# Kernel optimization log

Measured on AMD Instinct MI355X. Metric: run time of the kernel, lower is better.

Reference implementation:

```python
import jax, jax.numpy as jnp
import numpy as np

D_INNER = 1024
D_STATE = 16
DT_RANK = 64


def setup_inputs() -> dict:
    key = jax.random.key(0)
    k1, k2, k3, k4 = jax.random.split(key, 4)
    B, T = 8, 2048
    x = jax.random.normal(k1, (B, T, D_INNER), dtype=jnp.float32)
    pad_mask = jnp.zeros((B, T), dtype=bool)
    # nn.Linear weights: out = x @ W.T
    Wxp = 0.02 * jax.random.normal(k2, (DT_RANK + 2 * D_STATE, D_INNER), dtype=jnp.float32)
    Wdt = 0.02 * jax.random.normal(k3, (D_INNER, DT_RANK), dtype=jnp.float32)
    bdt = 0.02 * jax.random.normal(k4, (D_INNER,), dtype=jnp.float32)
    # log_A init: log(arange(1..d_state)) expanded to (d_inner, d_state)
    log_A = jnp.broadcast_to(jnp.log(jnp.arange(1, D_STATE + 1, dtype=jnp.float32))[None, :],
                             (D_INNER, D_STATE)).copy()
    D_param = jnp.ones((D_INNER,), dtype=jnp.float32)
    return {"x": x, "pad_mask": pad_mask, "Wxp": Wxp, "Wdt": Wdt, "bdt": bdt,
            "log_A": log_A, "D_param": D_param}


def reference(x, pad_mask, Wxp, Wdt, bdt, log_A, D_param):
    B, T, Din = x.shape
    xp = jnp.einsum('btd,kd->btk', x, Wxp)                      # (B,T,dt_rank+2N)
    dt = jax.nn.softplus(jnp.einsum('btr,dr->btd', xp[..., :DT_RANK], Wdt) + bdt)  # (B,T,Din)
    B_seq = xp[..., DT_RANK:DT_RANK + D_STATE]                  # (B,T,N)
    C_seq = xp[..., DT_RANK + D_STATE:]                         # (B,T,N)
    A = -jnp.exp(log_A)                                         # (Din,N)
    mask = (~pad_mask).astype(x.dtype)                          # (B,T), 1 = keep

    def step(h, inp):
        dt_t, B_t, C_t, x_t, m = inp   # (B,Din),(B,N),(B,N),(B,Din),(B,)
        dA = jnp.exp(A[None] * dt_t[..., None])                 # (B,Din,N)
        h = dA * h + (dt_t * x_t)[..., None] * B_t[:, None, :]  # (B,Din,N)
        y = jnp.einsum('bdn,bn->bd', h, C_t) + D_param * x_t
        y = y * m[:, None]
        h = h * m[:, None, None]
        return h, y

    h0 = jnp.zeros((B, Din, D_STATE), x.dtype)
    xs = (jnp.swapaxes(dt, 0, 1), jnp.swapaxes(B_seq, 0, 1),
          jnp.swapaxes(C_seq, 0, 1), jnp.swapaxes(x, 0, 1), mask.T)
    _, ys = jax.lax.scan(step, h0, xs)                          # ys: (T,B,Din)
    return jnp.swapaxes(ys, 0, 1)
```

## Files before the change

### kernel.cpp

```cpp
#include <hip/hip_runtime.h>
#include <stdint.h>

#define DIN 1024
#define TLEN 2048
#define NCH 16
#define CHT 128
#define WIN 32

typedef __attribute__((ext_vector_type(8))) short bf16x8;
typedef __attribute__((ext_vector_type(4))) float f32x4;

__device__ __forceinline__ short f2bf_trunc(float f) {
  union { float f; uint32_t u; } v; v.f = f;
  return (short)(v.u >> 16);
}
__device__ __forceinline__ short f2bf_rne(float f) {
  union { float f; uint32_t u; } v; v.f = f;
  uint32_t r = v.u + 0x7FFFu + ((v.u >> 16) & 1u);
  return (short)(r >> 16);
}
__device__ __forceinline__ float bf2f(short s) {
  union { uint32_t u; float f; } v; v.u = ((uint32_t)(unsigned short)s) << 16;
  return v.f;
}
__device__ __forceinline__ uint32_t pack_bf2(float a, float b) {
  union { float f; uint32_t u; } va, vb; va.f = a; vb.f = b;
  return (va.u >> 16) | (vb.u & 0xFFFF0000u);
}
__device__ __forceinline__ float softplus_f(float v) {
  float e = __builtin_amdgcn_exp2f(v * 1.44269504f);
  float sp = __builtin_amdgcn_logf(1.0f + e) * 0.6931471806f;
  return v > 15.0f ? v : sp;
}
__device__ __forceinline__ void gl_lds16(const void* g, void* l) {
  __builtin_amdgcn_global_load_lds(
      (const __attribute__((address_space(1))) uint32_t*)g,
      (__attribute__((address_space(3))) uint32_t*)l, 16, 0, 0);
}
__device__ __forceinline__ f32x4 mfma16(bf16x8 a, bf16x8 b, f32x4 c) {
  return __builtin_amdgcn_mfma_f32_16x16x32_bf16(a, b, c, 0, 0, 0);
}
template <int CTRL>
__device__ __forceinline__ float dpp_add(float v) {
  int r = __builtin_amdgcn_update_dpp(0, __builtin_bit_cast(int, v), CTRL, 0xF, 0xF, 0);
  return v + __builtin_bit_cast(float, r);
}

__global__ void k_prep(const float* __restrict__ Wxp, const float* __restrict__ Wdt,
                       const float* __restrict__ logA, const unsigned char* __restrict__ pad,
                       short* __restrict__ wxp_bf, short* __restrict__ wdt_bf,
                       float* __restrict__ al2, uint32_t* __restrict__ padbits) {
  int i = blockIdx.x * 256 + threadIdx.x;
  if (i < 96 * 1024) wxp_bf[i] = f2bf_rne(Wxp[i]);
  if (i < 1024 * 64) wdt_bf[i] = f2bf_rne(Wdt[i]);
  if (i < 1024 * 16) al2[i] = -__expf(logA[i]) * 1.44269504f;
  if (i < 512) {
    uint32_t m = 0;
    const unsigned char* p = pad + (size_t)i * 32;
    for (int j = 0; j < 32; ++j) m |= (p[j] ? 1u : 0u) << j;
    padbits[i] = m;
  }
}

__global__ __launch_bounds__(256) void k_proj(
    const float* __restrict__ x, const short* __restrict__ wxp_bf,
    short* __restrict__ xp_dt, float* __restrict__ BC) {
  const int w = threadIdx.x >> 6, l = threadIdx.x & 63;
  const int cl = l & 15, q = l >> 4, kb = q * 8;
  const int rh = w & 1, ch = w >> 1;
  const int xrow = blockIdx.x * 32 + rh * 16 + cl;

  f32x4 acc[3];
#pragma unroll
  for (int t = 0; t < 3; ++t) acc[t] = (f32x4){0.f, 0.f, 0.f, 0.f};

  const float* xr = x + (size_t)xrow * DIN + kb;
  const short* wb = wxp_bf + (size_t)(ch * 48 + cl) * DIN + kb;
#pragma unroll 2
  for (int k0 = 0; k0 < DIN; k0 += 32) {
    float4 p0 = *(const float4*)(xr + k0);
    float4 p1 = *(const float4*)(xr + k0 + 4);
    bf16x8 xb;
    xb[0] = f2bf_trunc(p0.x); xb[1] = f2bf_trunc(p0.y);
    xb[2] = f2bf_trunc(p0.z); xb[3] = f2bf_trunc(p0.w);
    xb[4] = f2bf_trunc(p1.x); xb[5] = f2bf_trunc(p1.y);
    xb[6] = f2bf_trunc(p1.z); xb[7] = f2bf_trunc(p1.w);
#pragma unroll
    for (int t = 0; t < 3; ++t) {
      bf16x8 wf = *(const bf16x8*)(wb + (size_t)t * 16 * DIN + k0);
      acc[t] = mfma16(wf, xb, acc[t]);
    }
  }
#pragma unroll
  for (int t = 0; t < 3; ++t) {
    int oc = ch * 48 + t * 16 + q * 4;
    if (oc < 64) {
      uint2 uu;
      uu.x = pack_bf2(acc[t][0], acc[t][1]);
      uu.y = pack_bf2(acc[t][2], acc[t][3]);
      *(uint2*)(xp_dt + (size_t)xrow * 64 + oc) = uu;
    } else {
      *(f32x4*)(BC + (size_t)xrow * 32 + (oc - 64)) = acc[t];
    }
  }
}

__global__ __launch_bounds__(256) void k_scan1(
    const float* __restrict__ x, const float* __restrict__ BC,
    const short* __restrict__ xp_dt, const short* __restrict__ wdt_bf,
    const float* __restrict__ bdt, const float* __restrict__ al2,
    const float* __restrict__ Dparam, const uint32_t* __restrict__ padbits,
    float* __restrict__ Y, float* __restrict__ Ssum, short* __restrict__ Hfin) {
  __shared__ float x_w[2][33 * 64];
  __shared__ float bc_w[2][33 * 32];
  __shared__ float dt_w[2][33 * 68];

  const int tid = threadIdx.x;
  const int w = tid >> 6, l = tid & 63;
  const int cl = l & 15, q = l >> 4, kb = q * 8;
  const int dg = blockIdx.x & 15;
  const int chunk = (blockIdx.x >> 4) & 15;
  const int b = blockIdx.x >> 8;
  const int d0 = dg * 64;
  const int cb = chunk * CHT;
  const int grp = tid >> 2, l2 = tid & 3, n0 = l2 * 4;
  const int d = d0 + grp;

  const f32x4 cA = *(const f32x4*)(al2 + (size_t)d * 16 + n0);
  const float Dp = Dparam[d];

  const int th = w & 1, dh = w >> 1;
  const short* wr0 = wdt_bf + (size_t)(d0 + dh * 32 + cl) * 64 + kb;
  const short* wr1 = wdt_bf + (size_t)(d0 + dh * 32 + 16 + cl) * 64 + kb;
  bf16x8 aw00 = *(const bf16x8*)(wr0);
  bf16x8 aw01 = *(const bf16x8*)(wr0 + 32);
  bf16x8 aw10 = *(const bf16x8*)(wr1);
  bf16x8 aw11 = *(const bf16x8*)(wr1 + 32);
  f32x4 bias0 = *(const f32x4*)(bdt + d0 + dh * 32 + q * 4);
  f32x4 bias1 = *(const f32x4*)(bdt + d0 + dh * 32 + 16 + q * 4);

  float h[4] = {0.f, 0.f, 0.f, 0.f};
  float S = 0.f;

  auto stage = [&](int t0, int buf) {
    const float* xg = x + ((size_t)(b * TLEN + t0)) * DIN + d0;
#pragma unroll
    for (int r = 0; r < 2; ++r) {
      int flat = r * 1024 + w * 256 + l * 4;
      int tt = flat >> 6, cc = flat & 63;
      gl_lds16(xg + (size_t)tt * DIN + cc, &x_w[buf][r * 1024 + w * 256]);
    }
    const float* bg = BC + ((size_t)(b * TLEN + t0)) * 32;
    gl_lds16(bg + w * 256 + l * 4, &bc_w[buf][w * 256]);
  };

  auto dtc = [&](int t0, int buf) {
    uint32_t mw = padbits[b * 64 + (t0 >> 5)];
    int tloc = th * 16 + cl;
    bool masked = (mw >> tloc) & 1;
    const short* ag = xp_dt + (size_t)(b * TLEN + t0 + tloc) * 64 + kb;
    bf16x8 b0 = *(const bf16x8*)(ag);
    bf16x8 b1 = *(const bf16x8*)(ag + 32);
    f32x4 ac = mfma16(aw00, b0, (f32x4){0.f, 0.f, 0.f, 0.f});
    ac = mfma16(aw01, b1, ac);
    f32x4 dv;
#pragma unroll
    for (int i = 0; i < 4; ++i) {
      float sp = softplus_f(ac[i] + bias0[i]);
      dv[i] = masked ? 1e9f : sp;
    }
    *(f32x4*)&dt_w[buf][tloc * 68 + dh * 32 + q * 4] = dv;
    ac = mfma16(aw10, b0, (f32x4){0.f, 0.f, 0.f, 0.f});
    ac = mfma16(aw11, b1, ac);
#pragma unroll
    for (int i = 0; i < 4; ++i) {
      float sp = softplus_f(ac[i] + bias1[i]);
      dv[i] = masked ? 1e9f : sp;
    }
    *(f32x4*)&dt_w[buf][tloc * 68 + dh * 32 + 16 + q * 4] = dv;
  };

  stage(cb, 0);
  dtc(cb, 0);
  __syncthreads();

  for (int win = 0; win < CHT / WIN; ++win) {
    const int curb = win & 1;
    const int t0 = cb + win * WIN;
    if (win < CHT / WIN - 1) { stage(t0 + WIN, curb ^ 1); dtc(t0 + WIN, curb ^ 1); }

    float* ybase = Y + ((size_t)(b * TLEN + t0)) * DIN + d;
    float dtv = dt_w[curb][grp];
    float xv = x_w[curb][grp];
    f32x4 Bv = *(const f32x4*)&bc_w[curb][n0];
    f32x4 Cv = *(const f32x4*)&bc_w[curb][16 + n0];
#pragma unroll 8
    for (int tt = 0; tt < WIN; ++tt) {
      float dtv_n = dt_w[curb][(tt + 1) * 68 + grp];
      float xv_n = x_w[curb][(tt + 1) * 64 + grp];
      f32x4 Bv_n = *(const f32x4*)&bc_w[curb][(tt + 1) * 32 + n0];
      f32x4 Cv_n = *(const f32x4*)&bc_w[curb][(tt + 1) * 32 + 16 + n0];

      bool live = dtv < 1e8f;
      float dtx = live ? dtv * xv : 0.f;
#pragma unroll
      for (int n = 0; n < 4; ++n) {
        float e = __builtin_amdgcn_exp2f(cA[n] * dtv);
        h[n] = fmaf(e, h[n], dtx * Bv[n]);
      }
      float p = h[0] * Cv[0];
      p = fmaf(h[1], Cv[1], p);
      p = fmaf(h[2], Cv[2], p);
      p = fmaf(h[3], Cv[3], p);
      p = dpp_add<0xB1>(p);
      p = dpp_add<0x4E>(p);
      S += dtv;
      float yv = live ? fmaf(Dp, xv, p) : 0.f;
      if (l2 == 0) ybase[(size_t)tt * DIN] = yv;

      dtv = dtv_n; xv = xv_n; Bv = Bv_n; Cv = Cv_n;
    }
    __syncthreads();
  }

  if (l2 == 0) Ssum[(size_t)(b * NCH + chunk) * 1024 + d] = S;
  short4 hs;
  hs.x = f2bf_rne(h[0]); hs.y = f2bf_rne(h[1]);
  hs.z = f2bf_rne(h[2]); hs.w = f2bf_rne(h[3]);
  *(short4*)(Hfin + ((size_t)(b * NCH + chunk) * 1024 + d) * 16 + n0) = hs;
}

__global__ __launch_bounds__(256) void k_fix(
    const float* __restrict__ BC, const short* __restrict__ xp_dt,
    const short* __restrict__ wdt_bf, const float* __restrict__ bdt,
    const float* __restrict__ al2, const uint32_t* __restrict__ padbits,
    const float* __restrict__ Ssum, const short* __restrict__ Hfin,
    float* __restrict__ Y) {
  __shared__ float dtw[32 * 260];
  __shared__ float c_w[32 * 16];

  const int tid = threadIdx.x;
  const int w = tid >> 6, l = tid & 63;
  const int cl = l & 15, q = l >> 4, kb = q * 8;
  const int b = blockIdx.x / 60;
  const int rem = blockIdx.x % 60;
  const int chunk = (rem >> 2) + 1;
  const int dblk = rem & 3;
  const int d = dblk * 256 + tid;
  const int th = w & 1, dh = w >> 1;

  float cA[16], hin[16];
#pragma unroll
  for (int g = 0; g < 4; ++g)
    *(f32x4*)&cA[g * 4] = *(const f32x4*)(al2 + (size_t)d * 16 + g * 4);
#pragma unroll
  for (int n = 0; n < 16; ++n) hin[n] = 0.f;

  for (int c = 0; c < chunk; ++c) {
    float s = Ssum[(size_t)(b * NCH + c) * 1024 + d];
    const short4* hp = (const short4*)(Hfin + ((size_t)(b * NCH + c) * 1024 + d) * 16);
#pragma unroll
    for (int g = 0; g < 4; ++g) {
      short4 hv = hp[g];
      hin[g * 4 + 0] = fmaf(__builtin_amdgcn_exp2f(cA[g * 4 + 0] * s), hin[g * 4 + 0], bf2f(hv.x));
      hin[g * 4 + 1] = fmaf(__builtin_amdgcn_exp2f(cA[g * 4 + 1] * s), hin[g * 4 + 1], bf2f(hv.y));
      hin[g * 4 + 2] = fmaf(__builtin_amdgcn_exp2f(cA[g * 4 + 2] * s), hin[g * 4 + 2], bf2f(hv.z));
      hin[g * 4 + 3] = fmaf(__builtin_amdgcn_exp2f(cA[g * 4 + 3] * s), hin[g * 4 + 3], bf2f(hv.w));
    }
  }

  float S = 0.f;
  for (int win = 0; win < CHT / WIN; ++win) {
    const int t0 = chunk * CHT + win * WIN;
    __syncthreads();
    if (w == 0) {
      gl_lds16(BC + ((size_t)(b * TLEN + t0 + (l >> 2))) * 32 + 16 + (l & 3) * 4, &c_w[0]);
      gl_lds16(BC + ((size_t)(b * TLEN + t0 + 16 + (l >> 2))) * 32 + 16 + (l & 3) * 4, &c_w[256]);
    }
    uint32_t mw = padbits[b * 64 + (t0 >> 5)];
    const int tloc = th * 16 + cl;
    const bool masked = (mw >> tloc) & 1;
    const short* ag = xp_dt + (size_t)(b * TLEN + t0 + tloc) * 64 + kb;
    bf16x8 xb0 = *(const bf16x8*)(ag);
    bf16x8 xb1 = *(const bf16x8*)(ag + 32);
#pragma unroll
    for (int dti = 0; dti < 8; ++dti) {
      int dd = dh * 128 + dti * 16;
      const short* wr = wdt_bf + (size_t)(dblk * 256 + dd + cl) * 64 + kb;
      bf16x8 a0 = *(const bf16x8*)(wr);
      bf16x8 a1 = *(const bf16x8*)(wr + 32);
      f32x4 ac = mfma16(a0, xb0, (f32x4){0.f, 0.f, 0.f, 0.f});
      ac = mfma16(a1, xb1, ac);
      f32x4 bv = *(const f32x4*)(bdt + dblk * 256 + dd + q * 4);
      f32x4 dv;
#pragma unroll
      for (int i = 0; i < 4; ++i) {
        float sp = softplus_f(ac[i] + bv[i]);
        dv[i] = masked ? 1e9f : sp;
      }
      *(f32x4*)&dtw[tloc * 260 + dd + q * 4] = dv;
    }
    __syncthreads();

    float* yb = Y + ((size_t)(b * TLEN + t0)) * DIN + d;
#pragma unroll
    for (int g = 0; g < 4; ++g) {
      float yv[8], de[8];
#pragma unroll
      for (int i = 0; i < 8; ++i) yv[i] = yb[(size_t)(g * 8 + i) * DIN];
#pragma unroll
      for (int i = 0; i < 8; ++i) de[i] = dtw[(g * 8 + i) * 260 + tid];
#pragma unroll
      for (int i = 0; i < 8; ++i) {
        S += de[i];
        float fix = 0.f;
        const f32x4* Ct = (const f32x4*)&c_w[(g * 8 + i) * 16];
#pragma unroll
        for (int n4 = 0; n4 < 4; ++n4) {
          f32x4 cv = Ct[n4];
#pragma unroll
          for (int j = 0; j < 4; ++j) {
            float e = __builtin_amdgcn_exp2f(cA[n4 * 4 + j] * S);
            fix = fmaf(e * cv[j], hin[n4 * 4 + j], fix);
          }
        }
        yv[i] += fix;
      }
#pragma unroll
      for (int i = 0; i < 8; ++i) yb[(size_t)(g * 8 + i) * DIN] = yv[i];
    }
  }
}

extern "C" void kernel_launch(void* const* d_in, const int* in_sizes, int n_in,
                              void* d_out, int out_size, void* d_ws, size_t ws_size,
                              hipStream_t stream) {
  const float* x = (const float*)d_in[0];
  const unsigned char* pad = (const unsigned char*)d_in[1];
  const float* Wxp = (const float*)d_in[2];
  const float* Wdt = (const float*)d_in[3];
  const float* bdt = (const float*)d_in[4];
  const float* logA = (const float*)d_in[5];
  const float* Dpar = (const float*)d_in[6];
  float* Y = (float*)d_out;

  char* ws = (char*)d_ws;
  short* wxp_bf    = (short*)(ws);
  short* wdt_bf    = (short*)(ws + 196608);
  float* al2       = (float*)(ws + 327680);
  short* xp_dt     = (short*)(ws + 393216);
  float* BC        = (float*)(ws + 2490368);
  float* Ssum      = (float*)(ws + 4587520);
  short* Hfin      = (short*)(ws + 5111808);
  uint32_t* padbits= (uint32_t*)(ws + 9306112);

  hipLaunchKernelGGL(k_prep, dim3(384), dim3(256), 0, stream,
                     Wxp, Wdt, logA, pad, wxp_bf, wdt_bf, al2, padbits);
  hipLaunchKernelGGL(k_proj, dim3(512), dim3(256), 0, stream,
                     x, wxp_bf, xp_dt, BC);
  hipLaunchKernelGGL(k_scan1, dim3(2048), dim3(256), 0, stream,
                     x, BC, xp_dt, wdt_bf, bdt, al2, Dpar, padbits, Y, Ssum, Hfin);
  hipLaunchKernelGGL(k_fix, dim3(480), dim3(256), 0, stream,
                     BC, xp_dt, wdt_bf, bdt, al2, padbits, Ssum, Hfin, Y);
}
```

Measured before the change: 274.2 us.

## Restructure chunked scan into state pass, carry combine, and seeded output pass

Replaces the scan-plus-fixup scheme with three stages. A state-only chunk scan writes the final states and dt sums, a small kernel combines the carries across chunks, and a second scan starts from the correct initial state and writes Y directly. This removes the fix kernel's read-modify-write of Y and its recomputation of dt, at the cost of scanning x twice. Separately, the projection now stages x through swizzled LDS with double buffering, and dt is held in LDS as bf16 with round-to-nearest-even packing, which adds some rounding risk.

```diff
diff --git a/kernel.cpp b/kernel.cpp
--- a/kernel.cpp
+++ b/kernel.cpp
@@ -23,9 +23,8 @@
   union { uint32_t u; float f; } v; v.u = ((uint32_t)(unsigned short)s) << 16;
   return v.f;
 }
-__device__ __forceinline__ uint32_t pack_bf2(float a, float b) {
-  union { float f; uint32_t u; } va, vb; va.f = a; vb.f = b;
-  return (va.u >> 16) | (vb.u & 0xFFFF0000u);
+__device__ __forceinline__ uint32_t pack_bf2_rne(float a, float b) {
+  return (uint32_t)(uint16_t)f2bf_rne(a) | ((uint32_t)(uint16_t)f2bf_rne(b) << 16);
 }
 __device__ __forceinline__ float softplus_f(float v) {
   float e = __builtin_amdgcn_exp2f(v * 1.44269504f);
@@ -65,39 +64,60 @@
 __global__ __launch_bounds__(256) void k_proj(
     const float* __restrict__ x, const short* __restrict__ wxp_bf,
     short* __restrict__ xp_dt, float* __restrict__ BC) {
-  const int w = threadIdx.x >> 6, l = threadIdx.x & 63;
+  __shared__ float xs[2][32 * 64];
+  const int tid = threadIdx.x;
+  const int w = tid >> 6, l = tid & 63;
   const int cl = l & 15, q = l >> 4, kb = q * 8;
-  const int rh = w & 1, ch = w >> 1;
-  const int xrow = blockIdx.x * 32 + rh * 16 + cl;
+  const int rt = w & 1, ch3 = w >> 1;
+  const int row0 = blockIdx.x * 32;
 
   f32x4 acc[3];
 #pragma unroll
   for (int t = 0; t < 3; ++t) acc[t] = (f32x4){0.f, 0.f, 0.f, 0.f};
 
-  const float* xr = x + (size_t)xrow * DIN + kb;
-  const short* wb = wxp_bf + (size_t)(ch * 48 + cl) * DIN + kb;
-#pragma unroll 2
-  for (int k0 = 0; k0 < DIN; k0 += 32) {
-    float4 p0 = *(const float4*)(xr + k0);
-    float4 p1 = *(const float4*)(xr + k0 + 4);
-    bf16x8 xb;
-    xb[0] = f2bf_trunc(p0.x); xb[1] = f2bf_trunc(p0.y);
-    xb[2] = f2bf_trunc(p0.z); xb[3] = f2bf_trunc(p0.w);
-    xb[4] = f2bf_trunc(p1.x); xb[5] = f2bf_trunc(p1.y);
-    xb[6] = f2bf_trunc(p1.z); xb[7] = f2bf_trunc(p1.w);
-#pragma unroll
-    for (int t = 0; t < 3; ++t) {
-      bf16x8 wf = *(const bf16x8*)(wb + (size_t)t * 16 * DIN + k0);
-      acc[t] = mfma16(wf, xb, acc[t]);
-    }
-  }
+  auto stage = [&](int k0, int buf) {
+#pragma unroll
+    for (int r = 0; r < 2; ++r) {
+      int flat = r * 1024 + tid * 4;
+      int row = flat >> 6, c0 = flat & 63;
+      int swc = c0 ^ ((row & 15) << 2);
+      gl_lds16(x + (size_t)(row0 + row) * DIN + k0 + swc,
+               &xs[buf][r * 1024 + w * 256]);
+    }
+  };
+
+  stage(0, 0);
+  __syncthreads();
+  const int Xr = cl << 2;
+  for (int k0 = 0; k0 < DIN; k0 += 64) {
+    const int buf = (k0 >> 6) & 1;
+    if (k0 < DIN - 64) stage(k0 + 64, buf ^ 1);
+#pragma unroll
+    for (int kk = 0; kk < 64; kk += 32) {
+      const float* xr = &xs[buf][(rt * 16 + cl) * 64];
+      float4 fa = *(const float4*)&xr[(kk + kb) ^ Xr];
+      float4 fb = *(const float4*)&xr[(kk + kb + 4) ^ Xr];
+      bf16x8 xb;
+      xb[0] = f2bf_trunc(fa.x); xb[1] = f2bf_trunc(fa.y);
+      xb[2] = f2bf_trunc(fa.z); xb[3] = f2bf_trunc(fa.w);
+      xb[4] = f2bf_trunc(fb.x); xb[5] = f2bf_trunc(fb.y);
+      xb[6] = f2bf_trunc(fb.z); xb[7] = f2bf_trunc(fb.w);
+#pragma unroll
+      for (int t = 0; t < 3; ++t) {
+        bf16x8 wf = *(const bf16x8*)(wxp_bf + (size_t)(ch3 * 48 + t * 16 + cl) * DIN + k0 + kk + kb);
+        acc[t] = mfma16(wf, xb, acc[t]);
+      }
+    }
+    __syncthreads();
+  }
+  const int xrow = row0 + rt * 16 + cl;
 #pragma unroll
   for (int t = 0; t < 3; ++t) {
-    int oc = ch * 48 + t * 16 + q * 4;
+    int oc = ch3 * 48 + t * 16 + q * 4;
     if (oc < 64) {
       uint2 uu;
-      uu.x = pack_bf2(acc[t][0], acc[t][1]);
-      uu.y = pack_bf2(acc[t][2], acc[t][3]);
+      uu.x = pack_bf2_rne(acc[t][0], acc[t][1]);
+      uu.y = pack_bf2_rne(acc[t][2], acc[t][3]);
       *(uint2*)(xp_dt + (size_t)xrow * 64 + oc) = uu;
     } else {
       *(f32x4*)(BC + (size_t)xrow * 32 + (oc - 64)) = acc[t];
@@ -105,15 +125,15 @@
   }
 }
 
-__global__ __launch_bounds__(256) void k_scan1(
+__global__ __launch_bounds__(256) void k_sc1(
     const float* __restrict__ x, const float* __restrict__ BC,
     const short* __restrict__ xp_dt, const short* __restrict__ wdt_bf,
     const float* __restrict__ bdt, const float* __restrict__ al2,
-    const float* __restrict__ Dparam, const uint32_t* __restrict__ padbits,
-    float* __restrict__ Y, float* __restrict__ Ssum, short* __restrict__ Hfin) {
+    const uint32_t* __restrict__ padbits,
+    float* __restrict__ Ssum, short* __restrict__ Hio) {
   __shared__ float x_w[2][33 * 64];
-  __shared__ float bc_w[2][33 * 32];
-  __shared__ float dt_w[2][33 * 68];
+  __shared__ short dt_w[2][33 * 68];
+  __shared__ float b_w[2][33 * 16];
 
   const int tid = threadIdx.x;
   const int w = tid >> 6, l = tid & 63;
@@ -125,11 +145,10 @@
   const int cb = chunk * CHT;
   const int grp = tid >> 2, l2 = tid & 3, n0 = l2 * 4;
   const int d = d0 + grp;
+  const int th = w & 1, dh = w >> 1;
 
   const f32x4 cA = *(const f32x4*)(al2 + (size_t)d * 16 + n0);
-  const float Dp = Dparam[d];
-
-  const int th = w & 1, dh = w >> 1;
+
   const short* wr0 = wdt_bf + (size_t)(d0 + dh * 32 + cl) * 64 + kb;
   const short* wr1 = wdt_bf + (size_t)(d0 + dh * 32 + 16 + cl) * 64 + kb;
   bf16x8 aw00 = *(const bf16x8*)(wr0);
@@ -150,8 +169,11 @@
       int tt = flat >> 6, cc = flat & 63;
       gl_lds16(xg + (size_t)tt * DIN + cc, &x_w[buf][r * 1024 + w * 256]);
     }
-    const float* bg = BC + ((size_t)(b * TLEN + t0)) * 32;
-    gl_lds16(bg + w * 256 + l * 4, &bc_w[buf][w * 256]);
+    if (w < 2) {
+      int flat = w * 256 + l * 4;
+      int tt = flat >> 4, cc = flat & 15;
+      gl_lds16(BC + ((size_t)(b * TLEN + t0 + tt)) * 32 + cc, &b_w[buf][w * 256]);
+    }
   };
 
   auto dtc = [&](int t0, int buf) {
@@ -163,21 +185,21 @@
     bf16x8 b1 = *(const bf16x8*)(ag + 32);
     f32x4 ac = mfma16(aw00, b0, (f32x4){0.f, 0.f, 0.f, 0.f});
     ac = mfma16(aw01, b1, ac);
-    f32x4 dv;
-#pragma unroll
-    for (int i = 0; i < 4; ++i) {
-      float sp = softplus_f(ac[i] + bias0[i]);
-      dv[i] = masked ? 1e9f : sp;
-    }
-    *(f32x4*)&dt_w[buf][tloc * 68 + dh * 32 + q * 4] = dv;
+    uint2 uu;
+    float s0 = masked ? 1e9f : softplus_f(ac[0] + bias0[0]);
+    float s1 = masked ? 1e9f : softplus_f(ac[1] + bias0[1]);
+    float s2 = masked ? 1e9f : softplus_f(ac[2] + bias0[2]);
+    float s3 = masked ? 1e9f : softplus_f(ac[3] + bias0[3]);
+    uu.x = pack_bf2_rne(s0, s1); uu.y = pack_bf2_rne(s2, s3);
+    *(uint2*)&dt_w[buf][tloc * 68 + dh * 32 + q * 4] = uu;
     ac = mfma16(aw10, b0, (f32x4){0.f, 0.f, 0.f, 0.f});
     ac = mfma16(aw11, b1, ac);
-#pragma unroll
-    for (int i = 0; i < 4; ++i) {
-      float sp = softplus_f(ac[i] + bias1[i]);
-      dv[i] = masked ? 1e9f : sp;
-    }
-    *(f32x4*)&dt_w[buf][tloc * 68 + dh * 32 + 16 + q * 4] = dv;
+    s0 = masked ? 1e9f : softplus_f(ac[0] + bias1[0]);
+    s1 = masked ? 1e9f : softplus_f(ac[1] + bias1[1]);
+    s2 = masked ? 1e9f : softplus_f(ac[2] + bias1[2]);
+    s3 = masked ? 1e9f : softplus_f(ac[3] + bias1[3]);
+    uu.x = pack_bf2_rne(s0, s1); uu.y = pack_bf2_rne(s2, s3);
+    *(uint2*)&dt_w[buf][tloc * 68 + dh * 32 + 16 + q * 4] = uu;
   };
 
   stage(cb, 0);
@@ -189,14 +211,149 @@
     const int t0 = cb + win * WIN;
     if (win < CHT / WIN - 1) { stage(t0 + WIN, curb ^ 1); dtc(t0 + WIN, curb ^ 1); }
 
+    float dtv = bf2f(dt_w[curb][grp]);
+    float xv = x_w[curb][grp];
+    f32x4 Bv = *(const f32x4*)&b_w[curb][n0];
+#pragma unroll 8
+    for (int tt = 0; tt < WIN; ++tt) {
+      float dtv_n = bf2f(dt_w[curb][(tt + 1) * 68 + grp]);
+      float xv_n = x_w[curb][(tt + 1) * 64 + grp];
+      f32x4 Bv_n = *(const f32x4*)&b_w[curb][(tt + 1) * 16 + n0];
+
+      bool live = dtv < 1e8f;
+      float dtx = live ? dtv * xv : 0.f;
+#pragma unroll
+      for (int n = 0; n < 4; ++n) {
+        float e = __builtin_amdgcn_exp2f(cA[n] * dtv);
+        h[n] = fmaf(e, h[n], dtx * Bv[n]);
+      }
+      S += dtv;
+      dtv = dtv_n; xv = xv_n; Bv = Bv_n;
+    }
+    __syncthreads();
+  }
+
+  if (l2 == 0) Ssum[(size_t)(b * NCH + chunk) * 1024 + d] = S;
+  short4 hs;
+  hs.x = f2bf_rne(h[0]); hs.y = f2bf_rne(h[1]);
+  hs.z = f2bf_rne(h[2]); hs.w = f2bf_rne(h[3]);
+  *(short4*)(Hio + ((size_t)(b * NCH + chunk) * 1024 + d) * 16 + n0) = hs;
+}
+
+__global__ __launch_bounds__(256) void k_comb(
+    const float* __restrict__ al2, const float* __restrict__ Ssum,
+    short* __restrict__ Hio) {
+  int g = blockIdx.x * 256 + threadIdx.x;
+  int b = g >> 14;
+  int r = g & 16383;
+  int d = r >> 4;
+  const float cA = al2[r];
+  float H = 0.f;
+  for (int c = 0; c < NCH; ++c) {
+    size_t base = (size_t)(b * NCH + c) * 1024 + d;
+    float s = Ssum[base];
+    size_t idx = base * 16 + (r & 15);
+    float hf = bf2f(Hio[idx]);
+    float e = __builtin_amdgcn_exp2f(cA * s);
+    Hio[idx] = f2bf_rne(H);
+    H = fmaf(e, H, hf);
+  }
+}
+
+__global__ __launch_bounds__(256) void k_sc2(
+    const float* __restrict__ x, const float* __restrict__ BC,
+    const short* __restrict__ xp_dt, const short* __restrict__ wdt_bf,
+    const float* __restrict__ bdt, const float* __restrict__ al2,
+    const float* __restrict__ Dparam, const uint32_t* __restrict__ padbits,
+    const short* __restrict__ Hio, float* __restrict__ Y) {
+  __shared__ float x_w[2][33 * 64];
+  __shared__ short dt_w[2][33 * 68];
+  __shared__ float bc_w[2][33 * 32];
+
+  const int tid = threadIdx.x;
+  const int w = tid >> 6, l = tid & 63;
+  const int cl = l & 15, q = l >> 4, kb = q * 8;
+  const int dg = blockIdx.x & 15;
+  const int chunk = (blockIdx.x >> 4) & 15;
+  const int b = blockIdx.x >> 8;
+  const int d0 = dg * 64;
+  const int cb = chunk * CHT;
+  const int grp = tid >> 2, l2 = tid & 3, n0 = l2 * 4;
+  const int d = d0 + grp;
+  const int th = w & 1, dh = w >> 1;
+
+  const f32x4 cA = *(const f32x4*)(al2 + (size_t)d * 16 + n0);
+  const float Dp = Dparam[d];
+
+  const short* wr0 = wdt_bf + (size_t)(d0 + dh * 32 + cl) * 64 + kb;
+  const short* wr1 = wdt_bf + (size_t)(d0 + dh * 32 + 16 + cl) * 64 + kb;
+  bf16x8 aw00 = *(const bf16x8*)(wr0);
+  bf16x8 aw01 = *(const bf16x8*)(wr0 + 32);
+  bf16x8 aw10 = *(const bf16x8*)(wr1);
+  bf16x8 aw11 = *(const bf16x8*)(wr1 + 32);
+  f32x4 bias0 = *(const f32x4*)(bdt + d0 + dh * 32 + q * 4);
+  f32x4 bias1 = *(const f32x4*)(bdt + d0 + dh * 32 + 16 + q * 4);
+
+  float h[4];
+  {
+    short4 hi4 = *(const short4*)(Hio + ((size_t)(b * NCH + chunk) * 1024 + d) * 16 + n0);
+    h[0] = bf2f(hi4.x); h[1] = bf2f(hi4.y); h[2] = bf2f(hi4.z); h[3] = bf2f(hi4.w);
+  }
+
+  auto stage = [&](int t0, int buf) {
+    const float* xg = x + ((size_t)(b * TLEN + t0)) * DIN + d0;
+#pragma unroll
+    for (int r = 0; r < 2; ++r) {
+      int flat = r * 1024 + w * 256 + l * 4;
+      int tt = flat >> 6, cc = flat & 63;
+      gl_lds16(xg + (size_t)tt * DIN + cc, &x_w[buf][r * 1024 + w * 256]);
+    }
+    gl_lds16(BC + ((size_t)(b * TLEN + t0)) * 32 + w * 256 + l * 4, &bc_w[buf][w * 256]);
+  };
+
+  auto dtc = [&](int t0, int buf) {
+    uint32_t mw = padbits[b * 64 + (t0 >> 5)];
+    int tloc = th * 16 + cl;
+    bool masked = (mw >> tloc) & 1;
+    const short* ag = xp_dt + (size_t)(b * TLEN + t0 + tloc) * 64 + kb;
+    bf16x8 b0 = *(const bf16x8*)(ag);
+    bf16x8 b1 = *(const bf16x8*)(ag + 32);
+    f32x4 ac = mfma16(aw00, b0, (f32x4){0.f, 0.f, 0.f, 0.f});
+    ac = mfma16(aw01, b1, ac);
+    uint2 uu;
+    float s0 = masked ? 1e9f : softplus_f(ac[0] + bias0[0]);
+    float s1 = masked ? 1e9f : softplus_f(ac[1] + bias0[1]);
+    float s2 = masked ? 1e9f : softplus_f(ac[2] + bias0[2]);
+    float s3 = masked ? 1e9f : softplus_f(ac[3] + bias0[3]);
+    uu.x = pack_bf2_rne(s0, s1); uu.y = pack_bf2_rne(s2, s3);
+    *(uint2*)&dt_w[buf][tloc * 68 + dh * 32 + q * 4] = uu;
+    ac = mfma16(aw10, b0, (f32x4){0.f, 0.f, 0.f, 0.f});
+    ac = mfma16(aw11, b1, ac);
+    s0 = masked ? 1e9f : softplus_f(ac[0] + bias1[0]);
+    s1 = masked ? 1e9f : softplus_f(ac[1] + bias1[1]);
+    s2 = masked ? 1e9f : softplus_f(ac[2] + bias1[2]);
+    s3 = masked ? 1e9f : softplus_f(ac[3] + bias1[3]);
+    uu.x = pack_bf2_rne(s0, s1); uu.y = pack_bf2_rne(s2, s3);
+    *(uint2*)&dt_w[buf][tloc * 68 + dh * 32 + 16 + q * 4] = uu;
+  };
+
+  stage(cb, 0);
+  dtc(cb, 0);
+  __syncthreads();
+
+  for (int win = 0; win < CHT / WIN; ++win) {
+    const int curb = win & 1;
+    const int t0 = cb + win * WIN;
+    if (win < CHT / WIN - 1) { stage(t0 + WIN, curb ^ 1); dtc(t0 + WIN, curb ^ 1); }
+
     float* ybase = Y + ((size_t)(b * TLEN + t0)) * DIN + d;
-    float dtv = dt_w[curb][grp];
+    float dtv = bf2f(dt_w[curb][grp]);
     float xv = x_w[curb][grp];
     f32x4 Bv = *(const f32x4*)&bc_w[curb][n0];
     f32x4 Cv = *(const f32x4*)&bc_w[curb][16 + n0];
 #pragma unroll 8
     for (int tt = 0; tt < WIN; ++tt) {
-      float dtv_n = dt_w[curb][(tt + 1) * 68 + grp];
+      float dtv_n = bf2f(dt_w[curb][(tt + 1) * 68 + grp]);
       float xv_n = x_w[curb][(tt + 1) * 64 + grp];
       f32x4 Bv_n = *(const f32x4*)&bc_w[curb][(tt + 1) * 32 + n0];
       f32x4 Cv_n = *(const f32x4*)&bc_w[curb][(tt + 1) * 32 + 16 + n0];
@@ -214,121 +371,12 @@
       p = fmaf(h[3], Cv[3], p);
       p = dpp_add<0xB1>(p);
       p = dpp_add<0x4E>(p);
-      S += dtv;
       float yv = live ? fmaf(Dp, xv, p) : 0.f;
       if (l2 == 0) ybase[(size_t)tt * DIN] = yv;
 
       dtv = dtv_n; xv = xv_n; Bv = Bv_n; Cv = Cv_n;
     }
     __syncthreads();
-  }
-
-  if (l2 == 0) Ssum[(size_t)(b * NCH + chunk) * 1024 + d] = S;
-  short4 hs;
-  hs.x = f2bf_rne(h[0]); hs.y = f2bf_rne(h[1]);
-  hs.z = f2bf_rne(h[2]); hs.w = f2bf_rne(h[3]);
-  *(short4*)(Hfin + ((size_t)(b * NCH + chunk) * 1024 + d) * 16 + n0) = hs;
-}
-
-__global__ __launch_bounds__(256) void k_fix(
-    const float* __restrict__ BC, const short* __restrict__ xp_dt,
-    const short* __restrict__ wdt_bf, const float* __restrict__ bdt,
-    const float* __restrict__ al2, const uint32_t* __restrict__ padbits,
-    const float* __restrict__ Ssum, const short* __restrict__ Hfin,
-    float* __restrict__ Y) {
-  __shared__ float dtw[32 * 260];
-  __shared__ float c_w[32 * 16];
-
-  const int tid = threadIdx.x;
-  const int w = tid >> 6, l = tid & 63;
-  const int cl = l & 15, q = l >> 4, kb = q * 8;
-  const int b = blockIdx.x / 60;
-  const int rem = blockIdx.x % 60;
-  const int chunk = (rem >> 2) + 1;
-  const int dblk = rem & 3;
-  const int d = dblk * 256 + tid;
-  const int th = w & 1, dh = w >> 1;
-
-  float cA[16], hin[16];
-#pragma unroll
-  for (int g = 0; g < 4; ++g)
-    *(f32x4*)&cA[g * 4] = *(const f32x4*)(al2 + (size_t)d * 16 + g * 4);
-#pragma unroll
-  for (int n = 0; n < 16; ++n) hin[n] = 0.f;
-
-  for (int c = 0; c < chunk; ++c) {
-    float s = Ssum[(size_t)(b * NCH + c) * 1024 + d];
-    const short4* hp = (const short4*)(Hfin + ((size_t)(b * NCH + c) * 1024 + d) * 16);
-#pragma unroll
-    for (int g = 0; g < 4; ++g) {
-      short4 hv = hp[g];
-      hin[g * 4 + 0] = fmaf(__builtin_amdgcn_exp2f(cA[g * 4 + 0] * s), hin[g * 4 + 0], bf2f(hv.x));
-      hin[g * 4 + 1] = fmaf(__builtin_amdgcn_exp2f(cA[g * 4 + 1] * s), hin[g * 4 + 1], bf2f(hv.y));
-      hin[g * 4 + 2] = fmaf(__builtin_amdgcn_exp2f(cA[g * 4 + 2] * s), hin[g * 4 + 2], bf2f(hv.z));
-      hin[g * 4 + 3] = fmaf(__builtin_amdgcn_exp2f(cA[g * 4 + 3] * s), hin[g * 4 + 3], bf2f(hv.w));
-    }
-  }
-
-  float S = 0.f;
-  for (int win = 0; win < CHT / WIN; ++win) {
-    const int t0 = chunk * CHT + win * WIN;
-    __syncthreads();
-    if (w == 0) {
-      gl_lds16(BC + ((size_t)(b * TLEN + t0 + (l >> 2))) * 32 + 16 + (l & 3) * 4, &c_w[0]);
-      gl_lds16(BC + ((size_t)(b * TLEN + t0 + 16 + (l >> 2))) * 32 + 16 + (l & 3) * 4, &c_w[256]);
-    }
-    uint32_t mw = padbits[b * 64 + (t0 >> 5)];
-    const int tloc = th * 16 + cl;
-    const bool masked = (mw >> tloc) & 1;
-    const short* ag = xp_dt + (size_t)(b * TLEN + t0 + tloc) * 64 + kb;
-    bf16x8 xb0 = *(const bf16x8*)(ag);
-    bf16x8 xb1 = *(const bf16x8*)(ag + 32);
-#pragma unroll
-    for (int dti = 0; dti < 8; ++dti) {
-      int dd = dh * 128 + dti * 16;
-      const short* wr = wdt_bf + (size_t)(dblk * 256 + dd + cl) * 64 + kb;
-      bf16x8 a0 = *(const bf16x8*)(wr);
-      bf16x8 a1 = *(const bf16x8*)(wr + 32);
-      f32x4 ac = mfma16(a0, xb0, (f32x4){0.f, 0.f, 0.f, 0.f});
-      ac = mfma16(a1, xb1, ac);
-      f32x4 bv = *(const f32x4*)(bdt + dblk * 256 + dd + q * 4);
-      f32x4 dv;
-#pragma unroll
-      for (int i = 0; i < 4; ++i) {
-        float sp = softplus_f(ac[i] + bv[i]);
-        dv[i] = masked ? 1e9f : sp;
-      }
-      *(f32x4*)&dtw[tloc * 260 + dd + q * 4] = dv;
-    }
-    __syncthreads();
-
-    float* yb = Y + ((size_t)(b * TLEN + t0)) * DIN + d;
-#pragma unroll
-    for (int g = 0; g < 4; ++g) {
-      float yv[8], de[8];
-#pragma unroll
-      for (int i = 0; i < 8; ++i) yv[i] = yb[(size_t)(g * 8 + i) * DIN];
-#pragma unroll
-      for (int i = 0; i < 8; ++i) de[i] = dtw[(g * 8 + i) * 260 + tid];
-#pragma unroll
-      for (int i = 0; i < 8; ++i) {
-        S += de[i];
-        float fix = 0.f;
-        const f32x4* Ct = (const f32x4*)&c_w[(g * 8 + i) * 16];
-#pragma unroll
-        for (int n4 = 0; n4 < 4; ++n4) {
-          f32x4 cv = Ct[n4];
-#pragma unroll
-          for (int j = 0; j < 4; ++j) {
-            float e = __builtin_amdgcn_exp2f(cA[n4 * 4 + j] * S);
-            fix = fmaf(e * cv[j], hin[n4 * 4 + j], fix);
-          }
-        }
-        yv[i] += fix;
-      }
-#pragma unroll
-      for (int i = 0; i < 8; ++i) yb[(size_t)(g * 8 + i) * DIN] = yv[i];
-    }
   }
 }
 
@@ -345,21 +393,23 @@
   float* Y = (float*)d_out;
 
   char* ws = (char*)d_ws;
-  short* wxp_bf    = (short*)(ws);
-  short* wdt_bf    = (short*)(ws + 196608);
-  float* al2       = (float*)(ws + 327680);
-  short* xp_dt     = (short*)(ws + 393216);
-  float* BC        = (float*)(ws + 2490368);
-  float* Ssum      = (float*)(ws + 4587520);
-  short* Hfin      = (short*)(ws + 5111808);
-  uint32_t* padbits= (uint32_t*)(ws + 9306112);
+  short* wxp_bf     = (short*)(ws);
+  short* wdt_bf     = (short*)(ws + 196608);
+  float* al2        = (float*)(ws + 327680);
+  short* xp_dt      = (short*)(ws + 393216);
+  float* BC         = (float*)(ws + 2490368);
+  float* Ssum       = (float*)(ws + 4587520);
+  short* Hio        = (short*)(ws + 5111808);
+  uint32_t* padbits = (uint32_t*)(ws + 9306112);
 
   hipLaunchKernelGGL(k_prep, dim3(384), dim3(256), 0, stream,
                      Wxp, Wdt, logA, pad, wxp_bf, wdt_bf, al2, padbits);
   hipLaunchKernelGGL(k_proj, dim3(512), dim3(256), 0, stream,
                      x, wxp_bf, xp_dt, BC);
-  hipLaunchKernelGGL(k_scan1, dim3(2048), dim3(256), 0, stream,
-                     x, BC, xp_dt, wdt_bf, bdt, al2, Dpar, padbits, Y, Ssum, Hfin);
-  hipLaunchKernelGGL(k_fix, dim3(480), dim3(256), 0, stream,
-                     BC, xp_dt, wdt_bf, bdt, al2, padbits, Ssum, Hfin, Y);
-}
+  hipLaunchKernelGGL(k_sc1, dim3(2048), dim3(256), 0, stream,
+                     x, BC, xp_dt, wdt_bf, bdt, al2, padbits, Ssum, Hio);
+  hipLaunchKernelGGL(k_comb, dim3(512), dim3(256), 0, stream,
+                     al2, Ssum, Hio);
+  hipLaunchKernelGGL(k_sc2, dim3(2048), dim3(256), 0, stream,
+                     x, BC, xp_dt, wdt_bf, bdt, al2, Dpar, padbits, Hio, Y);
+}
```

Result: faster. 260.0 us (-5.2%).
